# Kernel tuning notes

Measured on AMD Instinct MI355X. Metric: run time of the kernel, lower is better.

Reference implementation:

```python
import jax, jax.numpy as jnp
import numpy as np

DOWN = 2
KCONV = 3

def _blur_kernel():
    # _setup_kernel([1,3,3,1]): outer product, normalize; is_ref flips it.
    k = np.array([1.0, 3.0, 3.0, 1.0], dtype=np.float32)
    K = np.outer(k, k)
    K /= K.sum()
    K = K[::-1, ::-1].copy()  # torch.flip(dims=(0,1)) (symmetric here, kept for fidelity)
    return jnp.asarray(K)  # [4,4]

def setup_inputs() -> dict:
    key = jax.random.key(0)
    k1, k2, k3 = jax.random.split(key, 3)
    x = jax.random.normal(k1, (16, 256, 128, 128), dtype=jnp.float32)
    weight = jax.random.normal(k2, (512, 256, KCONV, KCONV), dtype=jnp.float32)  # OIHW
    bias = jax.random.normal(k3, (512,), dtype=jnp.float32)
    return {"x": x, "weight": weight, "bias": bias, "blur_k": _blur_kernel()}

def reference(x, weight, bias, blur_k):
    N, C, H, W = x.shape
    Wb = blur_k.shape[-1]
    # pad sizes: p = Wb - down + (Wconv - 1)
    p = Wb - DOWN + (KCONV - 1)
    pad0, pad1 = (p + 1) // 2, p // 2
    # upfirdn_2d (up=down=1): pad + depthwise FIR correlation with the (pre-flipped) kernel
    kd = jnp.broadcast_to(blur_k[None, None], (C, 1, Wb, Wb))  # depthwise OIHW
    xb = jax.lax.conv_general_dilated(
        x, kd, window_strides=(1, 1),
        padding=[(pad0, pad1), (pad0, pad1)],
        feature_group_count=C,
        dimension_numbers=("NCHW", "OIHW", "NCHW"))  # [N,C,129,129]
    # EqualizedLRConv2d: runtime weight scaling 1/sqrt(fan_in), stride=2, no padding
    fan_in = weight.shape[1] * weight.shape[2] * weight.shape[3]
    scale = 1.0 / np.sqrt(fan_in)
    y = jax.lax.conv_general_dilated(
        xb, weight * jnp.float32(scale), window_strides=(DOWN, DOWN),
        padding="VALID",
        dimension_numbers=("NCHW", "OIHW", "NCHW"))  # [N,512,64,64]
    return y + bias[None, :, None, None]
```

## Files before the change

kernel.cpp:

```cpp
#include <hip/hip_runtime.h>
#include <hip/hip_bf16.h>
#include <stdint.h>
#include <stddef.h>

#define NB   16
#define CIN  256
#define HIN  128
#define WIN  128
#define COUT 512
#define HO   64
#define WO   64
#define HBL  129

typedef __attribute__((ext_vector_type(8))) __bf16 bf16x8;
typedef __attribute__((ext_vector_type(4))) float  f32x4;

__device__ __forceinline__ void gld_lds16(const void* g, void* l) {
  __builtin_amdgcn_global_load_lds(
      (const __attribute__((address_space(1))) void*)g,
      (__attribute__((address_space(3))) void*)l, 16, 0, 0);
}

__device__ __forceinline__ unsigned pack_bf16(float lo, float hi) {
  __hip_bfloat16 l = __float2bfloat16(lo), h = __float2bfloat16(hi);
  unsigned short ul = *(unsigned short*)&l, uh = *(unsigned short*)&h;
  return (unsigned)ul | ((unsigned)uh << 16);
}

__global__ __launch_bounds__(512) void blur_kernel(
    const float* __restrict__ x,
    const float* __restrict__ bk,
    __hip_bfloat16* __restrict__ xb)
{
  __shared__ __hip_bfloat16 lout[CIN * 130];

  const int bid0 = blockIdx.x;
  const int bid  = (bid0 & 7) * 258 + (bid0 >> 3);
  const int n    = bid / HBL;
  const int io   = bid % HBL;
  const int t    = threadIdx.x;
  const int wave = t >> 6;
  const int lane = t & 63;
  const int half = lane >> 5;
  const int g    = lane & 31;

  const float K11 = bk[5];
  float a[4], b[4];
  #pragma unroll
  for (int u = 0; u < 4; ++u) a[u] = bk[u * 4 + 1] / K11;
  #pragma unroll
  for (int v = 0; v < 4; ++v) b[v] = bk[4 + v];

  int rr[4];
  #pragma unroll
  for (int u = 0; u < 4; ++u) {
    int r = io - 2 + u;
    if (r < 0 || r >= HIN) { a[u] = 0.f; r = 0; }
    rr[u] = r;
  }

  #pragma unroll 2
  for (int cb = wave * 2; cb < CIN; cb += 16) {
    const int c = cb + half;
    const float4* xr = (const float4*)(x + ((size_t)(n * CIN + c) * HIN) * WIN);
    float4 vm = {0.f, 0.f, 0.f, 0.f};
    #pragma unroll
    for (int u = 0; u < 4; ++u) {
      const float4 rv = xr[rr[u] * 32 + g];
      vm.x += a[u] * rv.x; vm.y += a[u] * rv.y;
      vm.z += a[u] * rv.z; vm.w += a[u] * rv.w;
    }
    float vmm2 = __shfl_up(vm.z, 1);
    float vmm1 = __shfl_up(vm.w, 1);
    float vmp4 = __shfl_down(vm.x, 1);
    if (g == 0)  { vmm2 = 0.f; vmm1 = 0.f; }
    if (g == 31) { vmp4 = 0.f; }
    const float o0 = b[0]*vmm2 + b[1]*vmm1 + b[2]*vm.x + b[3]*vm.y;
    const float o1 = b[0]*vmm1 + b[1]*vm.x + b[2]*vm.y + b[3]*vm.z;
    const float o2 = b[0]*vm.x + b[1]*vm.y + b[2]*vm.z + b[3]*vm.w;
    const float o3 = b[0]*vm.y + b[1]*vm.z + b[2]*vm.w + b[3]*vmp4;
    unsigned* dst = (unsigned*)&lout[c * 130 + 4 * g];
    dst[0] = pack_bf16(o0, o1);
    dst[1] = pack_bf16(o2, o3);
    if (g == 31)
      lout[c * 130 + 128] = __float2bfloat16(b[0]*vm.z + b[1]*vm.w);
  }

  __syncthreads();

  const size_t obase = ((size_t)(n * HBL + io)) * HBL * CIN;
  for (int e = t; e < 65 * 64; e += 512) {
    const int jp = e >> 6;
    const int l  = e & 63;
    const unsigned r0 = *(const unsigned*)&lout[(4*l + 0) * 130 + 2*jp];
    const unsigned r1 = *(const unsigned*)&lout[(4*l + 1) * 130 + 2*jp];
    const unsigned r2 = *(const unsigned*)&lout[(4*l + 2) * 130 + 2*jp];
    const unsigned r3 = *(const unsigned*)&lout[(4*l + 3) * 130 + 2*jp];
    uint2 s0, s1;
    s0.x = (r0 & 0xffffu) | (r1 << 16);
    s0.y = (r2 & 0xffffu) | (r3 << 16);
    s1.x = (r0 >> 16) | (r1 & 0xffff0000u);
    s1.y = (r2 >> 16) | (r3 & 0xffff0000u);
    *(uint2*)&xb[obase + (size_t)(2*jp) * CIN + 4*l] = s0;
    if (jp < 64)
      *(uint2*)&xb[obase + (size_t)(2*jp + 1) * CIN + 4*l] = s1;
  }
}

__global__ __launch_bounds__(256) void wprep_kernel(
    const float* __restrict__ w,
    __hip_bfloat16* __restrict__ wt)
{
  const int idx = blockIdx.x * 256 + threadIdx.x;
  if (idx >= 9 * COUT * CIN) return;
  const int c   = idx & (CIN - 1);
  const int o   = (idx >> 8) & (COUT - 1);
  const int tap = idx >> 17;
  wt[idx] = __float2bfloat16(w[(o * CIN + c) * 9 + tap]);
}

__global__ __launch_bounds__(512, 2) void gemm_kernel(
    const __hip_bfloat16* __restrict__ xb,
    const __hip_bfloat16* __restrict__ wt,
    const float* __restrict__ bias,
    float* __restrict__ y)
{
  __shared__ __align__(16) char lds[4 * 32768];

  const int t    = threadIdx.x;
  const int wave = t >> 6;
  const int lane = t & 63;
  const int bid0 = blockIdx.x;
  const int bid  = (bid0 & 7) * 64 + (bid0 >> 3);
  const int nb   = bid & 1;
  const int mb   = bid >> 1;
  const int o0   = nb * 256;
  const int p0   = mb * 256;
  const int imgn = p0 >> 12;
  const int h0   = (p0 >> 6) & 63;

  const int wo  = wave >> 2;
  const int wp  = wave & 3;
  const int q   = lane >> 4;
  const int m16 = lane & 15;

  long xg[2], wg[2];
  int  ldsoff[2];
  #pragma unroll
  for (int s = 0; s < 2; ++s) {
    const int ia = wave * 2 + s;
    const int Lr = ia * 8 + (lane >> 3);
    const int g3 = (lane & 7) ^ (Lr & 7);
    const int r  = 2 * Lr + (g3 >> 2);
    const int cq = (g3 & 3) * 8;
    const int hh = h0 + (r >> 6);
    const int ww = r & 63;
    xg[s] = ((long)(imgn * HBL + 2 * hh) * HBL + 2 * ww) * CIN + cq;
    wg[s] = (long)(o0 + r) * CIN + cq;
    ldsoff[s] = ia * 1024;
  }

  const int g3f   = (((m16 & 1) << 2) | q) ^ ((m16 >> 1) & 7);
  const int abase = ((wo * 128 + m16) >> 1) * 128 + g3f * 16;
  const int bbase = ((wp * 64  + m16) >> 1) * 128 + g3f * 16;

  f32x4 acc[8][4];
  #pragma unroll
  for (int of = 0; of < 8; ++of)
    #pragma unroll
    for (int pf = 0; pf < 4; ++pf)
      acc[of][pf] = (f32x4){0.f, 0.f, 0.f, 0.f};

  auto stage = [&](int kt) {
    const int  slot = kt & 3;
    const int  tap  = kt >> 3;
    const int  cb   = (kt & 7) * 32;
    const long xoff = (long)((tap / 3) * HBL + (tap % 3)) * CIN + cb;
    const long woff = (long)tap * (COUT * CIN) + cb;
    char* sb = &lds[slot * 32768];
    #pragma unroll
    for (int s = 0; s < 2; ++s) {
      gld_lds16(wt + woff + wg[s], sb + ldsoff[s]);
      gld_lds16(xb + xoff + xg[s], sb + 16384 + ldsoff[s]);
    }
  };

  auto read_frags = [&](bf16x8 (&aw)[8], bf16x8 (&bx)[4], const char* sb) {
    #pragma unroll
    for (int i = 0; i < 8; ++i)
      aw[i] = *(const bf16x8*)(sb + abase + i * 1024);
    #pragma unroll
    for (int i = 0; i < 4; ++i)
      bx[i] = *(const bf16x8*)(sb + 16384 + bbase + i * 1024);
  };

  auto mfma_tile = [&](const bf16x8 (&aw)[8], const bf16x8 (&bx)[4]) {
    __builtin_amdgcn_s_setprio(1);
    #pragma unroll
    for (int of = 0; of < 8; ++of)
      #pragma unroll
      for (int pf = 0; pf < 4; ++pf)
        acc[of][pf] = __builtin_amdgcn_mfma_f32_16x16x32_bf16(
            aw[of], bx[pf], acc[of][pf], 0, 0, 0);
    __builtin_amdgcn_s_setprio(0);
  };

  bf16x8 awA[8], bxA[4], awB[8], bxB[4];

  auto body = [&](int kt, bf16x8 (&cAW)[8], bf16x8 (&cBX)[4],
                  bf16x8 (&nAW)[8], bf16x8 (&nBX)[4]) {
    if (kt <= 68) stage(kt + 3);
    if (kt < 71)
      read_frags(nAW, nBX, &lds[((kt + 1) & 3) * 32768]);
    mfma_tile(cAW, cBX);
    asm volatile("s_waitcnt lgkmcnt(0)" ::: "memory");
    __builtin_amdgcn_sched_barrier(0);
    if (kt <= 68)      asm volatile("s_waitcnt vmcnt(4)" ::: "memory");
    else if (kt == 69) asm volatile("s_waitcnt vmcnt(0)" ::: "memory");
    __builtin_amdgcn_s_barrier();
    __builtin_amdgcn_sched_barrier(0);
  };

  stage(0); stage(1); stage(2);
  asm volatile("s_waitcnt vmcnt(4)" ::: "memory");
  __builtin_amdgcn_s_barrier();
  __builtin_amdgcn_sched_barrier(0);
  read_frags(awA, bxA, &lds[0]);
  asm volatile("s_waitcnt lgkmcnt(0)" ::: "memory");
  __builtin_amdgcn_sched_barrier(0);

  for (int ktp = 0; ktp < 72; ktp += 2) {
    body(ktp,     awA, bxA, awB, bxB);
    body(ktp + 1, awB, bxB, awA, bxA);
  }

  const float scale = 1.0f / 48.0f;
  #pragma unroll
  for (int of = 0; of < 8; ++of) {
    const int o = o0 + wo * 128 + of * 16 + q * 4;
    #pragma unroll
    for (int pf = 0; pf < 4; ++pf) {
      const int p  = p0 + wp * 64 + pf * 16 + m16;
      const int n  = p >> 12;
      const int hh = (p >> 6) & 63;
      const int ww = p & 63;
      const size_t obase = ((size_t)(n * COUT + o) * HO + hh) * WO + ww;
      #pragma unroll
      for (int rg = 0; rg < 4; ++rg) {
        const float v = acc[of][pf][rg] * scale + bias[o + rg];
        y[obase + (size_t)rg * (HO * WO)] = v;
      }
    }
  }
}

extern "C" void kernel_launch(void* const* d_in, const int* in_sizes, int n_in,
                              void* d_out, int out_size, void* d_ws, size_t ws_size,
                              hipStream_t stream) {
  const float* x  = (const float*)d_in[0];
  const float* w  = (const float*)d_in[1];
  const float* bs = (const float*)d_in[2];
  const float* bk = (const float*)d_in[3];
  float* y = (float*)d_out;

  __hip_bfloat16* xb = (__hip_bfloat16*)d_ws;
  __hip_bfloat16* wt = (__hip_bfloat16*)((char*)d_ws +
                       (size_t)NB * HBL * HBL * CIN * sizeof(__hip_bfloat16));

  hipLaunchKernelGGL(blur_kernel, dim3(NB * HBL), dim3(512), 0, stream, x, bk, xb);
  hipLaunchKernelGGL(wprep_kernel, dim3((9 * COUT * CIN + 255) / 256), dim3(256), 0, stream, w, wt);
  hipLaunchKernelGGL(gemm_kernel, dim3(256 * 2), dim3(512), 0, stream,
                     xb, wt, bs, y);
}
```

Baseline: 562.4 us.

## Restructure GEMM main loop into eight half-tile phases with split W/X staging

Result: no change. 562.7 us (+0.1%).

```diff
diff --git a/kernel.cpp b/kernel.cpp
--- a/kernel.cpp
+++ b/kernel.cpp
@@ -119,13 +119,50 @@
   wt[idx] = __float2bfloat16(w[(o * CIN + c) * 9 + tap]);
 }
 
+#define VMW(N) asm volatile("s_waitcnt vmcnt(" #N ")" ::: "memory")
+
+#define MFMA1(QH, I, J)                                                       \
+  acc[(QH)*4+(I)][(J)] = __builtin_amdgcn_mfma_f32_16x16x32_bf16(             \
+      a##I, bx##J, acc[(QH)*4+(I)][(J)], 0, 0, 0)
+
+#define PHASE(QH, DU, READB, STG, VMSTMT)                                     \
+  {                                                                           \
+    const int u_ = u0 + (DU);                                                 \
+    const char* sA = lds + ((u_ >> 1) & 1) * 65536 + (u_ & 1) * 16384;        \
+    const char* sB = sA + 32768;                                              \
+    bf16x8 a0 = *(const bf16x8*)(sA + abase + ((QH)*4 + 0) * 1024);           \
+    bf16x8 a1 = *(const bf16x8*)(sA + abase + ((QH)*4 + 1) * 1024);           \
+    bf16x8 a2 = *(const bf16x8*)(sA + abase + ((QH)*4 + 2) * 1024);           \
+    bf16x8 a3 = *(const bf16x8*)(sA + abase + ((QH)*4 + 3) * 1024);           \
+    if (READB) {                                                              \
+      bx0 = *(const bf16x8*)(sB + bbase + 0 * 1024);                          \
+      bx1 = *(const bf16x8*)(sB + bbase + 1 * 1024);                          \
+      bx2 = *(const bf16x8*)(sB + bbase + 2 * 1024);                          \
+      bx3 = *(const bf16x8*)(sB + bbase + 3 * 1024);                          \
+    }                                                                         \
+    STG;                                                                      \
+    VMSTMT;                                                                   \
+    __builtin_amdgcn_s_barrier();                                             \
+    asm volatile("s_waitcnt lgkmcnt(0)" ::: "memory");                        \
+    __builtin_amdgcn_sched_barrier(0);                                        \
+    __builtin_amdgcn_s_setprio(1);                                            \
+    MFMA1(QH,0,0); MFMA1(QH,0,1); MFMA1(QH,0,2); MFMA1(QH,0,3);               \
+    MFMA1(QH,1,0); MFMA1(QH,1,1); MFMA1(QH,1,2); MFMA1(QH,1,3);               \
+    MFMA1(QH,2,0); MFMA1(QH,2,1); MFMA1(QH,2,2); MFMA1(QH,2,3);               \
+    MFMA1(QH,3,0); MFMA1(QH,3,1); MFMA1(QH,3,2); MFMA1(QH,3,3);               \
+    __builtin_amdgcn_s_setprio(0);                                            \
+    __builtin_amdgcn_sched_barrier(0);                                        \
+    __builtin_amdgcn_s_barrier();                                             \
+    __builtin_amdgcn_sched_barrier(0);                                        \
+  }
+
 __global__ __launch_bounds__(512, 2) void gemm_kernel(
     const __hip_bfloat16* __restrict__ xb,
     const __hip_bfloat16* __restrict__ wt,
     const float* __restrict__ bias,
     float* __restrict__ y)
 {
-  __shared__ __align__(16) char lds[4 * 32768];
+  __shared__ __align__(16) char lds[2 * 65536];
 
   const int t    = threadIdx.x;
   const int wave = t >> 6;
@@ -171,67 +208,38 @@
     for (int pf = 0; pf < 4; ++pf)
       acc[of][pf] = (f32x4){0.f, 0.f, 0.f, 0.f};
 
-  auto stage = [&](int kt) {
-    const int  slot = kt & 3;
-    const int  tap  = kt >> 3;
-    const int  cb   = (kt & 7) * 32;
-    const long xoff = (long)((tap / 3) * HBL + (tap % 3)) * CIN + cb;
-    const long woff = (long)tap * (COUT * CIN) + cb;
-    char* sb = &lds[slot * 32768];
-    #pragma unroll
-    for (int s = 0; s < 2; ++s) {
-      gld_lds16(wt + woff + wg[s], sb + ldsoff[s]);
-      gld_lds16(xb + xoff + xg[s], sb + 16384 + ldsoff[s]);
-    }
+  auto stageW = [&](int u) {
+    const long woff = (long)(u >> 3) * (COUT * CIN) + (u & 7) * 32;
+    char* d = lds + ((u >> 1) & 1) * 65536 + (u & 1) * 16384;
+    gld_lds16(wt + woff + wg[0], d + ldsoff[0]);
+    gld_lds16(wt + woff + wg[1], d + ldsoff[1]);
   };
-
-  auto read_frags = [&](bf16x8 (&aw)[8], bf16x8 (&bx)[4], const char* sb) {
-    #pragma unroll
-    for (int i = 0; i < 8; ++i)
-      aw[i] = *(const bf16x8*)(sb + abase + i * 1024);
-    #pragma unroll
-    for (int i = 0; i < 4; ++i)
-      bx[i] = *(const bf16x8*)(sb + 16384 + bbase + i * 1024);
+  auto stageX = [&](int u) {
+    const int  tap = u >> 3;
+    const long xoff = (long)((tap / 3) * HBL + (tap % 3)) * CIN + (u & 7) * 32;
+    char* d = lds + ((u >> 1) & 1) * 65536 + 32768 + (u & 1) * 16384;
+    gld_lds16(xb + xoff + xg[0], d + ldsoff[0]);
+    gld_lds16(xb + xoff + xg[1], d + ldsoff[1]);
   };
 
-  auto mfma_tile = [&](const bf16x8 (&aw)[8], const bf16x8 (&bx)[4]) {
-    __builtin_amdgcn_s_setprio(1);
-    #pragma unroll
-    for (int of = 0; of < 8; ++of)
-      #pragma unroll
-      for (int pf = 0; pf < 4; ++pf)
-        acc[of][pf] = __builtin_amdgcn_mfma_f32_16x16x32_bf16(
-            aw[of], bx[pf], acc[of][pf], 0, 0, 0);
-    __builtin_amdgcn_s_setprio(0);
-  };
-
-  bf16x8 awA[8], bxA[4], awB[8], bxB[4];
-
-  auto body = [&](int kt, bf16x8 (&cAW)[8], bf16x8 (&cBX)[4],
-                  bf16x8 (&nAW)[8], bf16x8 (&nBX)[4]) {
-    if (kt <= 68) stage(kt + 3);
-    if (kt < 71)
-      read_frags(nAW, nBX, &lds[((kt + 1) & 3) * 32768]);
-    mfma_tile(cAW, cBX);
-    asm volatile("s_waitcnt lgkmcnt(0)" ::: "memory");
-    __builtin_amdgcn_sched_barrier(0);
-    if (kt <= 68)      asm volatile("s_waitcnt vmcnt(4)" ::: "memory");
-    else if (kt == 69) asm volatile("s_waitcnt vmcnt(0)" ::: "memory");
-    __builtin_amdgcn_s_barrier();
-    __builtin_amdgcn_sched_barrier(0);
-  };
-
-  stage(0); stage(1); stage(2);
-  asm volatile("s_waitcnt vmcnt(4)" ::: "memory");
+  stageX(0); stageW(0); stageX(1); stageW(1); stageX(2); stageW(2); stageX(3);
+  VMW(6);
   __builtin_amdgcn_s_barrier();
   __builtin_amdgcn_sched_barrier(0);
-  read_frags(awA, bxA, &lds[0]);
-  asm volatile("s_waitcnt lgkmcnt(0)" ::: "memory");
-  __builtin_amdgcn_sched_barrier(0);
-
-  for (int ktp = 0; ktp < 72; ktp += 2) {
-    body(ktp,     awA, bxA, awB, bxB);
-    body(ktp + 1, awB, bxB, awA, bxA);
+
+  bf16x8 bx0, bx1, bx2, bx3;
+
+  for (int i = 0; i < 18; ++i) {
+    const int u0 = 4 * i;
+    PHASE(0, 0, 1, stageW(u0 + 3),                     (void)0)
+    PHASE(1, 0, 0, if (u0 + 4 < 72) stageX(u0 + 4),    (void)0)
+    PHASE(0, 1, 1, if (u0 + 4 < 72) stageW(u0 + 4),    (void)0)
+    PHASE(1, 1, 0, if (u0 + 5 < 72) stageX(u0 + 5),
+          if (i < 17) { VMW(6); } else { VMW(0); })
+    PHASE(0, 2, 1, if (u0 + 5 < 72) stageW(u0 + 5),    (void)0)
+    PHASE(1, 2, 0, if (u0 + 6 < 72) stageX(u0 + 6),    (void)0)
+    PHASE(0, 3, 1, if (u0 + 6 < 72) stageW(u0 + 6),    (void)0)
+    PHASE(1, 3, 0, if (u0 + 7 < 72) stageX(u0 + 7),    VMW(6))
   }
 
   const float scale = 1.0f / 48.0f;
```
